# Performance work log

Measured on AMD Instinct MI355X. Metric: run time of the kernel, lower is better.

Reference implementation:

```python
import jax, jax.numpy as jnp
import numpy as np
from jax.ops import segment_sum, segment_max

N, E = 50000, 500000
D_IN, D_H, D_OUT = 128, 256, 40
BN_EPS = 1e-5


def setup_inputs() -> dict:
    key = jax.random.key(0)
    ks = jax.random.split(key, 16)
    g = lambda k, shape, fan: jax.random.normal(k, shape, jnp.float32) * (1.0 / np.sqrt(fan))
    inp = {
        "x": jax.random.normal(ks[0], (N, D_IN), jnp.float32),
        "edge_index": jax.random.randint(ks[1], (2, E), 0, N, jnp.int64),
        # GAT (heads=1)
        "W_gat": g(ks[2], (D_IN, D_H), D_IN),
        "att_src": g(ks[3], (D_H,), D_H),
        "att_dst": g(ks[4], (D_H,), D_H),
        "b_gat": jnp.zeros((D_H,), jnp.float32),
        # GIN MLP
        "W_gin1": g(ks[5], (D_IN, D_H), D_IN),
        "b_gin1": jnp.zeros((D_H,), jnp.float32),
        "W_gin2": g(ks[6], (D_H, D_H), D_H),
        "b_gin2": jnp.zeros((D_H,), jnp.float32),
        # GCN
        "W_gcn": g(ks[7], (D_IN, D_H), D_IN),
        "b_gcn": jnp.zeros((D_H,), jnp.float32),
        # BatchNorm1d(3*hidden)
        "gamma": jnp.ones((3 * D_H,), jnp.float32),
        "beta": jnp.zeros((3 * D_H,), jnp.float32),
        # head
        "W_lin": g(ks[8], (3 * D_H, D_H), 3 * D_H),
        "b_lin": jnp.zeros((D_H,), jnp.float32),
        "W_lin2": g(ks[9], (D_H, D_OUT), D_H),
        "b_lin2": jnp.zeros((D_OUT,), jnp.float32),
    }
    return inp


def _forward(x, edge_index, W_gat, att_src, att_dst, b_gat, W_gin1, b_gin1,
             W_gin2, b_gin2, W_gcn, b_gcn, gamma, beta, W_lin, b_lin, W_lin2, b_lin2):
    n = x.shape[0]
    src, dst = edge_index[0], edge_index[1]
    loop = jnp.arange(n, dtype=src.dtype)
    src_sl = jnp.concatenate([src, loop])  # edges + self-loops (GAT/GCN)
    dst_sl = jnp.concatenate([dst, loop])

    # ---- GATConv (1 head), messages src -> dst, softmax over dst ----
    xs = x @ W_gat                                   # [N, H]
    a = jax.nn.leaky_relu(xs @ att_src, negative_slope=0.2) if False else None
    e = (xs @ att_src)[src_sl] + (xs @ att_dst)[dst_sl]   # [E+N]
    e = jax.nn.leaky_relu(e, negative_slope=0.2)
    m = segment_max(e, dst_sl, num_segments=n)
    w = jnp.exp(e - m[dst_sl])
    denom = segment_sum(w, dst_sl, num_segments=n)
    alpha = w / denom[dst_sl]
    x_gat = segment_sum(alpha[:, None] * xs[src_sl], dst_sl, num_segments=n) + b_gat

    # ---- GINConv (eps=0): MLP(x + sum_neighbors x_j) ----
    agg = segment_sum(x[src], dst, num_segments=n)
    h = x + agg
    x_gin = jax.nn.relu(h @ W_gin1 + b_gin1) @ W_gin2 + b_gin2

    # ---- GCNConv: symmetric normalization with self-loops ----
    deg = segment_sum(jnp.ones_like(dst_sl, dtype=x.dtype), dst_sl, num_segments=n)
    dis = jax.lax.rsqrt(jnp.maximum(deg, 1.0))  # deg >= 1 due to self-loops
    norm = dis[src_sl] * dis[dst_sl]
    xw = x @ W_gcn
    x_gcn = segment_sum(norm[:, None] * xw[src_sl], dst_sl, num_segments=n) + b_gcn

    # ---- concat -> BN (training-mode batch stats) -> ReLU -> MLP head ----
    xc = jnp.concatenate([x_gat, x_gin, x_gcn], axis=1)  # [N, 3H]
    mu = jnp.mean(xc, axis=0)
    var = jnp.mean((xc - mu) ** 2, axis=0)
    xb = (xc - mu) * jax.lax.rsqrt(var + BN_EPS) * gamma + beta
    h2 = jax.nn.relu(jax.nn.relu(xb) @ W_lin + b_lin)
    return h2 @ W_lin2 + b_lin2


def reference(x, edge_index, W_gat, att_src, att_dst, b_gat, W_gin1, b_gin1,
              W_gin2, b_gin2, W_gcn, b_gcn, gamma, beta, W_lin, b_lin, W_lin2, b_lin2):
    return _forward(x, edge_index, W_gat, att_src, att_dst, b_gat, W_gin1, b_gin1,
                    W_gin2, b_gin2, W_gcn, b_gcn, gamma, beta, W_lin, b_lin, W_lin2, b_lin2)
```

## Files before the change

### kernel.cpp

```cpp
#include <hip/hip_runtime.h>
#include <math.h>

#define NN 50000
#define NE 500000

typedef __attribute__((ext_vector_type(8))) short short8;
typedef __attribute__((ext_vector_type(4))) float f32x4;

__device__ __forceinline__ float leaky02(float x) { return x > 0.f ? x : 0.2f * x; }
__device__ __forceinline__ ushort f2b(float f) {
    uint u = __float_as_uint(f);
    u += 0x7fffu + ((u >> 16) & 1u);
    return (ushort)(u >> 16);
}
__device__ __forceinline__ float b2f(ushort h) { return __uint_as_float(((uint)h) << 16); }
__device__ __forceinline__ float b2f_lo(uint w) { return __uint_as_float(w << 16); }
__device__ __forceinline__ float b2f_hi(uint w) { return __uint_as_float(w & 0xffff0000u); }
__device__ __forceinline__ uint pack2(float a, float b) {
    return (uint)f2b(a) | ((uint)f2b(b) << 16);
}

__global__ void mm_wt(const float* __restrict__ W, ushort* __restrict__ Wt, int K, int Nc)
{
    int idx = blockIdx.x * 256 + threadIdx.x;
    if (idx >= K * Nc) return;
    int n = idx / K, k = idx - n * K;
    Wt[idx] = f2b(W[(size_t)k * Nc + n]);
}

__global__ void mm_attvec(const float* __restrict__ W, const float* __restrict__ as_,
                          const float* __restrict__ ad_, float* __restrict__ va, float* __restrict__ vd)
{
    int i = threadIdx.x;
    const float* vec = (i < 128) ? as_ : ad_;
    int k = i & 127;
    float s = 0.f;
    for (int j = 0; j < 256; ++j) s += W[(size_t)k * 256 + j] * vec[j];
    if (i < 128) va[k] = s; else vd[k] = s;
}

__global__ __launch_bounds__(256) void mm_cvt_es(const float* __restrict__ x,
                                                 const float* __restrict__ va, const float* __restrict__ vd,
                                                 ushort* __restrict__ xb,
                                                 float* __restrict__ es, float* __restrict__ ed)
{
    int node = blockIdx.x * 4 + (threadIdx.x >> 6);
    int lane = threadIdx.x & 63;
    if (node >= NN) return;
    float2 xv = *(const float2*)(x + (size_t)node * 128 + lane * 2);
    float2 a = *(const float2*)(va + lane * 2);
    float2 b = *(const float2*)(vd + lane * 2);
    *(uint*)(xb + (size_t)node * 128 + lane * 2) = pack2(xv.x, xv.y);
    float s = xv.x * a.x + xv.y * a.y;
    float d = xv.x * b.x + xv.y * b.y;
    #pragma unroll
    for (int off = 32; off; off >>= 1) {
        s += __shfl_down(s, off);
        d += __shfl_down(d, off);
    }
    if (lane == 0) { es[node] = s; ed[node] = d; }
}

__global__ void mm_count(const int* __restrict__ dst, int* __restrict__ deg)
{
    int e = blockIdx.x * 256 + threadIdx.x;
    if (e >= NE) return;
    atomicAdd(&deg[dst[e]], 1);
}

__global__ __launch_bounds__(256) void mm_scan1(const int* __restrict__ deg, int* __restrict__ part)
{
    __shared__ int red[256];
    int i = blockIdx.x * 256 + threadIdx.x;
    red[threadIdx.x] = (i < NN) ? deg[i] : 0;
    __syncthreads();
    for (int off = 128; off; off >>= 1) {
        if (threadIdx.x < off) red[threadIdx.x] += red[threadIdx.x + off];
        __syncthreads();
    }
    if (threadIdx.x == 0) part[blockIdx.x] = red[0];
}

__global__ __launch_bounds__(256) void mm_scan2(int* __restrict__ part, int nb)
{
    __shared__ int tile[256];
    int t = threadIdx.x;
    int v = (t < nb) ? part[t] : 0;
    tile[t] = v; __syncthreads();
    for (int off = 1; off < 256; off <<= 1) {
        int a = (t >= off) ? tile[t - off] : 0;
        __syncthreads();
        tile[t] += a;
        __syncthreads();
    }
    if (t < nb) part[t] = tile[t] - v;
}

__global__ __launch_bounds__(256) void mm_scan3(const int* __restrict__ deg, const int* __restrict__ part,
                                                int* __restrict__ row_ptr, int* __restrict__ cursor)
{
    __shared__ int tile[256];
    int t = threadIdx.x;
    int i = blockIdx.x * 256 + t;
    int v = (i < NN) ? deg[i] : 0;
    tile[t] = v; __syncthreads();
    for (int off = 1; off < 256; off <<= 1) {
        int a = (t >= off) ? tile[t - off] : 0;
        __syncthreads();
        tile[t] += a;
        __syncthreads();
    }
    if (i < NN) {
        int ex = part[blockIdx.x] + tile[t] - v;
        row_ptr[i] = ex;
        cursor[i] = ex;
    }
    if (i == 0) row_ptr[NN] = NE;
}

__global__ void mm_fill(const int* __restrict__ src, const int* __restrict__ dst,
                        int* __restrict__ cursor, int* __restrict__ csr_src)
{
    int e = blockIdx.x * 256 + threadIdx.x;
    if (e >= NE) return;
    int pos = atomicAdd(&cursor[dst[e]], 1);
    csr_src[pos] = src[e];
}

__global__ void mm_dis(const int* __restrict__ row_ptr, float* __restrict__ dis)
{
    int i = blockIdx.x * 256 + threadIdx.x;
    if (i >= NN) return;
    dis[i] = rsqrtf((float)(row_ptr[i + 1] - row_ptr[i] + 1));
}

__global__ __launch_bounds__(256) void mm_node_agg(
    const int* __restrict__ row_ptr, const int* __restrict__ csr_src,
    const float* __restrict__ es, const float* __restrict__ ed,
    const float* __restrict__ dis,
    const ushort* __restrict__ xb, ushort* __restrict__ aggb)
{
    int d = blockIdx.x * 4 + (threadIdx.x >> 6);
    int lane = threadIdx.x & 63;
    if (d >= NN) return;
    int start = row_ptr[d], end = row_ptr[d + 1];
    float edd = ed[d], disd = dis[d];
    float selfv = leaky02(es[d] + edd);

    int myidx = -1; float myl = -3.0e38f, mynw = 0.f;
    if (start + lane < end) {
        myidx = csr_src[start + lane];
        myl = leaky02(es[myidx] + edd);
        mynw = dis[myidx] * disd;
    }
    float lmax = fmaxf(selfv, myl);
    for (int e = start + 64 + lane; e < end; e += 64)
        lmax = fmaxf(lmax, leaky02(es[csr_src[e]] + edd));
    #pragma unroll
    for (int off = 1; off < 64; off <<= 1) lmax = fmaxf(lmax, __shfl_xor(lmax, off));
    float m = lmax;

    float lsum = (myidx >= 0) ? __expf(myl - m) : 0.f;
    if (lane == 0) lsum += __expf(selfv - m);
    for (int e = start + 64 + lane; e < end; e += 64)
        lsum += __expf(leaky02(es[csr_src[e]] + edd) - m);
    #pragma unroll
    for (int off = 1; off < 64; off <<= 1) lsum += __shfl_xor(lsum, off);
    float inv = 1.f / lsum;
    float myal = __expf(myl - m) * inv;

    float aself = __expf(selfv - m) * inv;
    float d2 = disd * disd;
    uint wself = *(const uint*)(xb + (size_t)d * 128 + lane * 2);
    float x0 = b2f_lo(wself), x1 = b2f_hi(wself);
    float gat0 = aself * x0, gat1 = aself * x1;
    float gin0 = x0, gin1 = x1;
    float gcn0 = d2 * x0, gcn1 = d2 * x1;

    for (int base = start; base < end; base += 64) {
        int cnt = min(64, end - base);
        int bidx; float bal, bnw;
        if (base == start) { bidx = myidx; bal = myal; bnw = mynw; }
        else {
            bidx = -1; bal = 0.f; bnw = 0.f;
            if (base + lane < end) {
                bidx = csr_src[base + lane];
                bal = __expf(leaky02(es[bidx] + edd) - m) * inv;
                bnw = dis[bidx] * disd;
            }
        }
        int j = 0;
        for (; j + 4 <= cnt; j += 4) {
            int   s0 = __shfl(bidx, j),     s1 = __shfl(bidx, j + 1);
            int   s2 = __shfl(bidx, j + 2), s3 = __shfl(bidx, j + 3);
            float a0 = __shfl(bal, j),      a1 = __shfl(bal, j + 1);
            float a2 = __shfl(bal, j + 2),  a3 = __shfl(bal, j + 3);
            float n0 = __shfl(bnw, j),      n1 = __shfl(bnw, j + 1);
            float n2 = __shfl(bnw, j + 2),  n3 = __shfl(bnw, j + 3);
            uint w0 = *(const uint*)(xb + (size_t)s0 * 128 + lane * 2);
            uint w1 = *(const uint*)(xb + (size_t)s1 * 128 + lane * 2);
            uint w2 = *(const uint*)(xb + (size_t)s2 * 128 + lane * 2);
            uint w3 = *(const uint*)(xb + (size_t)s3 * 128 + lane * 2);
            float p0, p1;
            p0 = b2f_lo(w0); p1 = b2f_hi(w0);
            gat0 += a0 * p0; gat1 += a0 * p1; gin0 += p0; gin1 += p1; gcn0 += n0 * p0; gcn1 += n0 * p1;
            p0 = b2f_lo(w1); p1 = b2f_hi(w1);
            gat0 += a1 * p0; gat1 += a1 * p1; gin0 += p0; gin1 += p1; gcn0 += n1 * p0; gcn1 += n1 * p1;
            p0 = b2f_lo(w2); p1 = b2f_hi(w2);
            gat0 += a2 * p0; gat1 += a2 * p1; gin0 += p0; gin1 += p1; gcn0 += n2 * p0; gcn1 += n2 * p1;
            p0 = b2f_lo(w3); p1 = b2f_hi(w3);
            gat0 += a3 * p0; gat1 += a3 * p1; gin0 += p0; gin1 += p1; gcn0 += n3 * p0; gcn1 += n3 * p1;
        }
        for (; j < cnt; ++j) {
            int   s0 = __shfl(bidx, j);
            float a0 = __shfl(bal, j);
            float n0 = __shfl(bnw, j);
            uint w0 = *(const uint*)(xb + (size_t)s0 * 128 + lane * 2);
            float p0 = b2f_lo(w0), p1 = b2f_hi(w0);
            gat0 += a0 * p0; gat1 += a0 * p1; gin0 += p0; gin1 += p1; gcn0 += n0 * p0; gcn1 += n0 * p1;
        }
    }
    ushort* orow = aggb + (size_t)d * 384;
    *(uint*)(orow + lane * 2)       = pack2(gat0, gat1);
    *(uint*)(orow + 128 + lane * 2) = pack2(gin0, gin1);
    *(uint*)(orow + 256 + lane * 2) = pack2(gcn0, gcn1);
}

__global__ __launch_bounds__(256) void mm_gemm_bf(
    const ushort* __restrict__ A, int lda, const ushort* __restrict__ Bt,
    const float* __restrict__ bias, float* __restrict__ stats,
    ushort* __restrict__ Cb, int ldc,
    int M, int K, int relu)
{
    __shared__ ushort lds[16384];
    const int tid = threadIdx.x;
    const int wave = tid >> 6, lane = tid & 63;
    const int row0 = blockIdx.x * 128;
    const int col0 = blockIdx.y * 128;

    int arow0 = min(row0 + wave * 16 + (lane >> 2), M - 1);
    int arow1 = min(row0 + 64 + wave * 16 + (lane >> 2), M - 1);
    int brow0 = col0 + wave * 16 + (lane >> 2);
    int brow1 = col0 + 64 + wave * 16 + (lane >> 2);
    const ushort* pa0 = A + (size_t)arow0 * lda + (lane & 3) * 8;
    const ushort* pa1 = A + (size_t)arow1 * lda + (lane & 3) * 8;
    const ushort* pb0 = Bt + (size_t)brow0 * K + (lane & 3) * 8;
    const ushort* pb1 = Bt + (size_t)brow1 * K + (lane & 3) * 8;
    const int wr = (wave >> 1) * 64, wc = (wave & 1) * 64;

    f32x4 zero = {0.f, 0.f, 0.f, 0.f};
    f32x4 acc[4][4];
    #pragma unroll
    for (int m = 0; m < 4; ++m)
        #pragma unroll
        for (int n = 0; n < 4; ++n) acc[m][n] = zero;

    const int nt = K >> 5;

#define STAGE_BF(bufi) { \
    ushort* Lb = lds + (bufi) * 8192; \
    __builtin_amdgcn_global_load_lds((const __attribute__((address_space(1))) void*)pa0, \
        (__attribute__((address_space(3))) void*)(Lb + wave * 512), 16, 0, 0); \
    __builtin_amdgcn_global_load_lds((const __attribute__((address_space(1))) void*)pa1, \
        (__attribute__((address_space(3))) void*)(Lb + 2048 + wave * 512), 16, 0, 0); \
    __builtin_amdgcn_global_load_lds((const __attribute__((address_space(1))) void*)pb0, \
        (__attribute__((address_space(3))) void*)(Lb + 4096 + wave * 512), 16, 0, 0); \
    __builtin_amdgcn_global_load_lds((const __attribute__((address_space(1))) void*)pb1, \
        (__attribute__((address_space(3))) void*)(Lb + 6144 + wave * 512), 16, 0, 0); \
    pa0 += 32; pa1 += 32; pb0 += 32; pb1 += 32; }

    STAGE_BF(0);
    __syncthreads();
    for (int t = 0; t < nt; ++t) {
        int cur = t & 1;
        if (t + 1 < nt) STAGE_BF(cur ^ 1);
        const ushort* As = lds + cur * 8192;
        const ushort* Bs = As + 4096;
        short8 a[4], b[4];
        #pragma unroll
        for (int m = 0; m < 4; ++m)
            a[m] = *(const short8*)&As[(wr + m * 16 + (lane & 15)) * 32 + (lane >> 4) * 8];
        #pragma unroll
        for (int n = 0; n < 4; ++n)
            b[n] = *(const short8*)&Bs[(wc + n * 16 + (lane & 15)) * 32 + (lane >> 4) * 8];
        #pragma unroll
        for (int m = 0; m < 4; ++m)
            #pragma unroll
            for (int n = 0; n < 4; ++n)
                acc[m][n] = __builtin_amdgcn_mfma_f32_16x16x32_bf16(a[m], b[n], acc[m][n], 0, 0, 0);
        if (t + 1 < nt) __syncthreads();
    }
#undef STAGE_BF

    #pragma unroll
    for (int n = 0; n < 4; ++n) {
        int col = col0 + wc + n * 16 + (lane & 15);
        float bb = bias ? bias[col] : 0.f;
        float s_acc = 0.f, q_acc = 0.f;
        #pragma unroll
        for (int m = 0; m < 4; ++m) {
            int rb = row0 + wr + m * 16 + (lane >> 4) * 4;
            #pragma unroll
            for (int r = 0; r < 4; ++r) {
                int row = rb + r;
                if (row < M) {
                    float v = acc[m][n][r] + bb;
                    if (relu) v = fmaxf(v, 0.f);
                    Cb[(size_t)row * ldc + col] = f2b(v);
                    s_acc += v; q_acc += v * v;
                }
            }
        }
        if (stats) {
            s_acc += __shfl_xor(s_acc, 16); q_acc += __shfl_xor(q_acc, 16);
            s_acc += __shfl_xor(s_acc, 32); q_acc += __shfl_xor(q_acc, 32);
            if (lane < 16) {
                unsafeAtomicAdd(&stats[col], s_acc);
                unsafeAtomicAdd(&stats[768 + col], q_acc);
            }
        }
    }
}

__device__ __forceinline__ uint4 bn_relu_pack(uint4 w, const float* __restrict__ sc,
                                              const float* __restrict__ sh, int c)
{
    float4 sc0 = *(const float4*)(sc + c), sc1 = *(const float4*)(sc + c + 4);
    float4 sh0 = *(const float4*)(sh + c), sh1 = *(const float4*)(sh + c + 4);
    uint4 o;
    o.x = pack2(fmaxf(b2f_lo(w.x) * sc0.x + sh0.x, 0.f), fmaxf(b2f_hi(w.x) * sc0.y + sh0.y, 0.f));
    o.y = pack2(fmaxf(b2f_lo(w.y) * sc0.z + sh0.z, 0.f), fmaxf(b2f_hi(w.y) * sc0.w + sh0.w, 0.f));
    o.z = pack2(fmaxf(b2f_lo(w.z) * sc1.x + sh1.x, 0.f), fmaxf(b2f_hi(w.z) * sc1.y + sh1.y, 0.f));
    o.w = pack2(fmaxf(b2f_lo(w.w) * sc1.z + sh1.z, 0.f), fmaxf(b2f_hi(w.w) * sc1.w + sh1.w, 0.f));
    return o;
}

__global__ __launch_bounds__(256) void mm_gemm_bn(
    const ushort* __restrict__ A, const ushort* __restrict__ Bt,
    const float* __restrict__ bias,
    const float* __restrict__ sc, const float* __restrict__ sh,
    ushort* __restrict__ Cb, int ldc, int M)
{
    const int K = 768, lda = 768;
    __shared__ ushort lds[16384];
    const int tid = threadIdx.x;
    const int wave = tid >> 6, lane = tid & 63;
    const int row0 = blockIdx.x * 128;
    const int col0 = blockIdx.y * 128;

    int arow0 = min(row0 + wave * 16 + (lane >> 2), M - 1);
    int arow1 = min(row0 + 64 + wave * 16 + (lane >> 2), M - 1);
    int brow0 = col0 + wave * 16 + (lane >> 2);
    int brow1 = col0 + 64 + wave * 16 + (lane >> 2);
    const ushort* pa0 = A + (size_t)arow0 * lda + (lane & 3) * 8;
    const ushort* pa1 = A + (size_t)arow1 * lda + (lane & 3) * 8;
    const ushort* pb0 = Bt + (size_t)brow0 * K + (lane & 3) * 8;
    const ushort* pb1 = Bt + (size_t)brow1 * K + (lane & 3) * 8;
    const int wr = (wave >> 1) * 64, wc = (wave & 1) * 64;

    f32x4 zero = {0.f, 0.f, 0.f, 0.f};
    f32x4 acc[4][4];
    #pragma unroll
    for (int m = 0; m < 4; ++m)
        #pragma unroll
        for (int n = 0; n < 4; ++n) acc[m][n] = zero;

    const int nt = K >> 5;

#define STAGE_B(bufi) { \
    ushort* Lb = lds + (bufi) * 8192; \
    __builtin_amdgcn_global_load_lds((const __attribute__((address_space(1))) void*)pb0, \
        (__attribute__((address_space(3))) void*)(Lb + 4096 + wave * 512), 16, 0, 0); \
    __builtin_amdgcn_global_load_lds((const __attribute__((address_space(1))) void*)pb1, \
        (__attribute__((address_space(3))) void*)(Lb + 6144 + wave * 512), 16, 0, 0); \
    pb0 += 32; pb1 += 32; }

    {
        STAGE_B(0);
        uint4 w0 = *(const uint4*)pa0; uint4 w1 = *(const uint4*)pa1;
        pa0 += 32; pa1 += 32;
        int c = (lane & 3) * 8;
        uint4 oa = bn_relu_pack(w0, sc, sh, c);
        uint4 ob = bn_relu_pack(w1, sc, sh, c);
        *(uint4*)(lds + wave * 512 + lane * 8) = oa;
        *(uint4*)(lds + 2048 + wave * 512 + lane * 8) = ob;
    }
    __syncthreads();

    for (int t = 0; t < nt; ++t) {
        int cur = t & 1;
        uint4 w0n, w1n; int cn = 0;
        bool more = (t + 1 < nt);
        if (more) {
            STAGE_B(cur ^ 1);
            w0n = *(const uint4*)pa0; w1n = *(const uint4*)pa1;
            pa0 += 32; pa1 += 32;
            cn = (t + 1) * 32 + (lane & 3) * 8;
        }
        const ushort* As = lds + cur * 8192;
        const ushort* Bs = As + 4096;
        short8 a[4], b[4];
        #pragma unroll
        for (int m = 0; m < 4; ++m)
            a[m] = *(const short8*)&As[(wr + m * 16 + (lane & 15)) * 32 + (lane >> 4) * 8];
        #pragma unroll
        for (int n = 0; n < 4; ++n)
            b[n] = *(const short8*)&Bs[(wc + n * 16 + (lane & 15)) * 32 + (lane >> 4) * 8];
        #pragma unroll
        for (int m = 0; m < 4; ++m)
            #pragma unroll
            for (int n = 0; n < 4; ++n)
                acc[m][n] = __builtin_amdgcn_mfma_f32_16x16x32_bf16(a[m], b[n], acc[m][n], 0, 0, 0);
        if (more) {
            ushort* Ln = lds + (cur ^ 1) * 8192;
            uint4 oa = bn_relu_pack(w0n, sc, sh, cn);
            uint4 ob = bn_relu_pack(w1n, sc, sh, cn);
            *(uint4*)(Ln + wave * 512 + lane * 8) = oa;
            *(uint4*)(Ln + 2048 + wave * 512 + lane * 8) = ob;
            __syncthreads();
        }
    }
#undef STAGE_B

    #pragma unroll
    for (int n = 0; n < 4; ++n) {
        int col = col0 + wc + n * 16 + (lane & 15);
        float bb = bias[col];
        #pragma unroll
        for (int m = 0; m < 4; ++m) {
            int rb = row0 + wr + m * 16 + (lane >> 4) * 4;
            #pragma unroll
            for (int r = 0; r < 4; ++r) {
                int row = rb + r;
                if (row < M)
                    Cb[(size_t)row * ldc + col] = f2b(fmaxf(acc[m][n][r] + bb, 0.f));
            }
        }
    }
}

__global__ void mm_bn_fin(const float* __restrict__ sums, const float* __restrict__ gamma,
                          const float* __restrict__ beta,
                          float* __restrict__ scale, float* __restrict__ shift)
{
    int c = blockIdx.x * 256 + threadIdx.x;
    if (c >= 768) return;
    float inv = 1.f / (float)NN;
    float mu = sums[c] * inv;
    float ex2 = sums[768 + c] * inv;
    float var = fmaxf(ex2 - mu * mu, 0.f);
    float rs = rsqrtf(var + 1e-5f);
    float sc = gamma[c] * rs;
    scale[c] = sc;
    shift[c] = beta[c] - mu * sc;
}

__global__ __launch_bounds__(256) void mm_head2(const ushort* __restrict__ h2b, const float* __restrict__ W2,
                                                const float* __restrict__ b2, float* __restrict__ out)
{
    __shared__ float Ws[256 * 40];
    for (int i = threadIdx.x; i < 256 * 40; i += 256) Ws[i] = W2[i];
    __syncthreads();
    int row = blockIdx.x * 32 + (threadIdx.x >> 3);
    int cg = (threadIdx.x & 7) * 5;
    if (row >= NN) return;
    const ushort* hr = h2b + (size_t)row * 256;
    float acc[5] = {0, 0, 0, 0, 0};
    for (int k = 0; k < 256; k += 8) {
        uint4 w = *(const uint4*)(hr + k);
        float a0 = b2f_lo(w.x), a1 = b2f_hi(w.x), a2 = b2f_lo(w.y), a3 = b2f_hi(w.y);
        float a4 = b2f_lo(w.z), a5 = b2f_hi(w.z), a6 = b2f_lo(w.w), a7 = b2f_hi(w.w);
        #pragma unroll
        for (int j = 0; j < 5; ++j) {
            acc[j] += a0 * Ws[(k + 0) * 40 + cg + j] + a1 * Ws[(k + 1) * 40 + cg + j]
                    + a2 * Ws[(k + 2) * 40 + cg + j] + a3 * Ws[(k + 3) * 40 + cg + j]
                    + a4 * Ws[(k + 4) * 40 + cg + j] + a5 * Ws[(k + 5) * 40 + cg + j]
                    + a6 * Ws[(k + 6) * 40 + cg + j] + a7 * Ws[(k + 7) * 40 + cg + j];
        }
    }
    #pragma unroll
    for (int j = 0; j < 5; ++j) out[(size_t)row * 40 + cg + j] = acc[j] + b2[cg + j];
}

extern "C" void kernel_launch(void* const* d_in, const int* in_sizes, int n_in,
                              void* d_out, int out_size, void* d_ws, size_t ws_size,
                              hipStream_t stream)
{
    const float* x      = (const float*)d_in[0];
    const int*   ei     = (const int*)d_in[1];
    const float* W_gat  = (const float*)d_in[2];
    const float* att_s  = (const float*)d_in[3];
    const float* att_d  = (const float*)d_in[4];
    const float* b_gat  = (const float*)d_in[5];
    const float* W_gin1 = (const float*)d_in[6];
    const float* b_gin1 = (const float*)d_in[7];
    const float* W_gin2 = (const float*)d_in[8];
    const float* b_gin2 = (const float*)d_in[9];
    const float* W_gcn  = (const float*)d_in[10];
    const float* b_gcn  = (const float*)d_in[11];
    const float* gamma  = (const float*)d_in[12];
    const float* beta   = (const float*)d_in[13];
    const float* W_lin  = (const float*)d_in[14];
    const float* b_lin  = (const float*)d_in[15];
    const float* W_lin2 = (const float*)d_in[16];
    const float* b_lin2 = (const float*)d_in[17];
    const int* src = ei;
    const int* dst = ei + NE;
    float* out = (float*)d_out;

    float* ws = (float*)d_ws;
    size_t off = 0;
    ushort* xb      = (ushort*)(ws + off); off += (size_t)NN * 64;
    ushort* aggb    = (ushort*)(ws + off); off += (size_t)NN * 192;
    ushort* hid_b   = (ushort*)(ws + off); off += (size_t)NN * 128;
    ushort* xcb     = (ushort*)(ws + off); off += (size_t)NN * 384;
    float* es       = ws + off; off += NN;
    float* ed       = ws + off; off += NN;
    float* dis      = ws + off; off += NN;
    float* va       = ws + off; off += 128;
    float* vd       = ws + off; off += 128;
    float* bnsum    = ws + off; off += 1536;
    float* bscale   = ws + off; off += 768;
    float* bshift   = ws + off; off += 768;
    ushort* wt_gat  = (ushort*)(ws + off); off += 128 * 256 / 2;
    ushort* wt_gin1 = (ushort*)(ws + off); off += 128 * 256 / 2;
    ushort* wt_gin2 = (ushort*)(ws + off); off += 256 * 256 / 2;
    ushort* wt_gcn  = (ushort*)(ws + off); off += 128 * 256 / 2;
    ushort* wt_lin  = (ushort*)(ws + off); off += 768 * 256 / 2;
    int* part       = (int*)(ws + off); off += 256;
    int* row_ptr    = (int*)(ws + off); off += NN + 1;
    int* cursor     = (int*)(ws + off); off += NN;
    int* csr_src    = (int*)(ws + off); off += NE;

    dim3 blk(256);
    dim3 gemm_grid((NN + 127) / 128, 2);
    const int NB = (NN + 255) / 256;

    hipMemsetAsync(bnsum, 0, 1536 * sizeof(float), stream);
    hipMemsetAsync(cursor, 0, NN * sizeof(int), stream);

    mm_wt<<<(128 * 256 + 255) / 256, blk, 0, stream>>>(W_gat, wt_gat, 128, 256);
    mm_wt<<<(128 * 256 + 255) / 256, blk, 0, stream>>>(W_gin1, wt_gin1, 128, 256);
    mm_wt<<<(256 * 256 + 255) / 256, blk, 0, stream>>>(W_gin2, wt_gin2, 256, 256);
    mm_wt<<<(128 * 256 + 255) / 256, blk, 0, stream>>>(W_gcn, wt_gcn, 128, 256);
    mm_wt<<<(768 * 256 + 255) / 256, blk, 0, stream>>>(W_lin, wt_lin, 768, 256);
    mm_attvec<<<1, blk, 0, stream>>>(W_gat, att_s, att_d, va, vd);

    mm_cvt_es<<<(NN + 3) / 4, blk, 0, stream>>>(x, va, vd, xb, es, ed);

    mm_count<<<(NE + 255) / 256, blk, 0, stream>>>(dst, cursor);
    mm_scan1<<<NB, blk, 0, stream>>>(cursor, part);
    mm_scan2<<<1, blk, 0, stream>>>(part, NB);
    mm_scan3<<<NB, blk, 0, stream>>>(cursor, part, row_ptr, cursor);
    mm_dis<<<(NN + 255) / 256, blk, 0, stream>>>(row_ptr, dis);
    mm_fill<<<(NE + 255) / 256, blk, 0, stream>>>(src, dst, cursor, csr_src);

    mm_node_agg<<<(NN + 3) / 4, blk, 0, stream>>>(row_ptr, csr_src, es, ed, dis, xb, aggb);

    mm_gemm_bf<<<gemm_grid, blk, 0, stream>>>(aggb,       384, wt_gat,  b_gat,  bnsum,       xcb,       768, NN, 128, 0);
    mm_gemm_bf<<<gemm_grid, blk, 0, stream>>>(aggb + 128, 384, wt_gin1, b_gin1, nullptr,     hid_b,     256, NN, 128, 1);
    mm_gemm_bf<<<gemm_grid, blk, 0, stream>>>(hid_b,      256, wt_gin2, b_gin2, bnsum + 256, xcb + 256, 768, NN, 256, 0);
    mm_gemm_bf<<<gemm_grid, blk, 0, stream>>>(aggb + 256, 384, wt_gcn,  b_gcn,  bnsum + 512, xcb + 512, 768, NN, 128, 0);

    mm_bn_fin<<<3, blk, 0, stream>>>(bnsum, gamma, beta, bscale, bshift);

    mm_gemm_bn<<<gemm_grid, blk, 0, stream>>>(xcb, wt_lin, b_lin, bscale, bshift, hid_b, 256, NN);
    mm_head2<<<(NN + 31) / 32, blk, 0, stream>>>(hid_b, W_lin2, b_lin2, out);
}
```

Before: 419.2 us.

## Batch three GEMMs into one launch and relax LDS pipeline barriers

Folds the GAT, GIN1 and GCN projection GEMMs into one grid-z-indexed launch, cutting launch overhead and tail effects. Both GEMM kernels replace __syncthreads with explicit partial s_waitcnt vmcnt(4) plus raw s_barrier, so the next tile's async LDS loads can stay in flight while the current tile computes. The BN GEMM also caches the scale and shift vectors in shared memory and issues the A-row global loads earlier. Hand-written waitcnt counts are fragile and must exactly match the number of outstanding loads, or the kernel reads stale LDS data.

```diff
diff --git a/kernel.cpp b/kernel.cpp
--- a/kernel.cpp
+++ b/kernel.cpp
@@ -226,13 +226,12 @@
     *(uint*)(orow + 256 + lane * 2) = pack2(gcn0, gcn1);
 }
 
-__global__ __launch_bounds__(256) void mm_gemm_bf(
+__device__ __forceinline__ void gemm_core(
     const ushort* __restrict__ A, int lda, const ushort* __restrict__ Bt,
     const float* __restrict__ bias, float* __restrict__ stats,
-    ushort* __restrict__ Cb, int ldc,
-    int M, int K, int relu)
-{
-    __shared__ ushort lds[16384];
+    ushort* __restrict__ Cb, int ldc, int M, int K, int relu,
+    ushort* lds)
+{
     const int tid = threadIdx.x;
     const int wave = tid >> 6, lane = tid & 63;
     const int row0 = blockIdx.x * 128;
@@ -257,7 +256,7 @@
 
     const int nt = K >> 5;
 
-#define STAGE_BF(bufi) { \
+#define STAGE_C(bufi) { \
     ushort* Lb = lds + (bufi) * 8192; \
     __builtin_amdgcn_global_load_lds((const __attribute__((address_space(1))) void*)pa0, \
         (__attribute__((address_space(3))) void*)(Lb + wave * 512), 16, 0, 0); \
@@ -269,11 +268,16 @@
         (__attribute__((address_space(3))) void*)(Lb + 6144 + wave * 512), 16, 0, 0); \
     pa0 += 32; pa1 += 32; pb0 += 32; pb1 += 32; }
 
-    STAGE_BF(0);
-    __syncthreads();
+    STAGE_C(0);
     for (int t = 0; t < nt; ++t) {
         int cur = t & 1;
-        if (t + 1 < nt) STAGE_BF(cur ^ 1);
+        if (t + 1 < nt) {
+            STAGE_C(cur ^ 1);
+            asm volatile("s_waitcnt vmcnt(4) lgkmcnt(0)" ::: "memory");
+        } else {
+            asm volatile("s_waitcnt vmcnt(0) lgkmcnt(0)" ::: "memory");
+        }
+        __builtin_amdgcn_s_barrier();
         const ushort* As = lds + cur * 8192;
         const ushort* Bs = As + 4096;
         short8 a[4], b[4];
@@ -288,9 +292,9 @@
             #pragma unroll
             for (int n = 0; n < 4; ++n)
                 acc[m][n] = __builtin_amdgcn_mfma_f32_16x16x32_bf16(a[m], b[n], acc[m][n], 0, 0, 0);
-        if (t + 1 < nt) __syncthreads();
-    }
-#undef STAGE_BF
+        if (t + 1 < nt) __builtin_amdgcn_s_barrier();
+    }
+#undef STAGE_C
 
     #pragma unroll
     for (int n = 0; n < 4; ++n) {
@@ -322,16 +326,37 @@
     }
 }
 
-__device__ __forceinline__ uint4 bn_relu_pack(uint4 w, const float* __restrict__ sc,
-                                              const float* __restrict__ sh, int c)
-{
-    float4 sc0 = *(const float4*)(sc + c), sc1 = *(const float4*)(sc + c + 4);
-    float4 sh0 = *(const float4*)(sh + c), sh1 = *(const float4*)(sh + c + 4);
+__global__ __launch_bounds__(256) void mm_gemm3(
+    const ushort* __restrict__ aggb,
+    const ushort* __restrict__ wt_gat, const ushort* __restrict__ wt_gin1, const ushort* __restrict__ wt_gcn,
+    const float* __restrict__ b_gat, const float* __restrict__ b_gin1, const float* __restrict__ b_gcn,
+    float* __restrict__ bnsum,
+    ushort* __restrict__ xcb, ushort* __restrict__ hid_b)
+{
+    __shared__ ushort lds[16384];
+    const ushort* A; const ushort* Bt; const float* bias; float* stats; ushort* Cb; int ldc; int relu;
+    if (blockIdx.z == 0)      { A = aggb;       Bt = wt_gat;  bias = b_gat;  stats = bnsum;       Cb = xcb;       ldc = 768; relu = 0; }
+    else if (blockIdx.z == 1) { A = aggb + 128; Bt = wt_gin1; bias = b_gin1; stats = nullptr;     Cb = hid_b;     ldc = 256; relu = 1; }
+    else                      { A = aggb + 256; Bt = wt_gcn;  bias = b_gcn;  stats = bnsum + 512; Cb = xcb + 512; ldc = 768; relu = 0; }
+    gemm_core(A, 384, Bt, bias, stats, Cb, ldc, NN, 128, relu, lds);
+}
+
+__global__ __launch_bounds__(256) void mm_gemm_bf(
+    const ushort* __restrict__ A, int lda, const ushort* __restrict__ Bt,
+    const float* __restrict__ bias, float* __restrict__ stats,
+    ushort* __restrict__ Cb, int ldc, int M, int K, int relu)
+{
+    __shared__ ushort lds[16384];
+    gemm_core(A, lda, Bt, bias, stats, Cb, ldc, M, K, relu, lds);
+}
+
+__device__ __forceinline__ uint4 bn_relu_pack_l(uint4 w, const float* sc, const float* sh, int c)
+{
     uint4 o;
-    o.x = pack2(fmaxf(b2f_lo(w.x) * sc0.x + sh0.x, 0.f), fmaxf(b2f_hi(w.x) * sc0.y + sh0.y, 0.f));
-    o.y = pack2(fmaxf(b2f_lo(w.y) * sc0.z + sh0.z, 0.f), fmaxf(b2f_hi(w.y) * sc0.w + sh0.w, 0.f));
-    o.z = pack2(fmaxf(b2f_lo(w.z) * sc1.x + sh1.x, 0.f), fmaxf(b2f_hi(w.z) * sc1.y + sh1.y, 0.f));
-    o.w = pack2(fmaxf(b2f_lo(w.w) * sc1.z + sh1.z, 0.f), fmaxf(b2f_hi(w.w) * sc1.w + sh1.w, 0.f));
+    o.x = pack2(fmaxf(b2f_lo(w.x) * sc[c + 0] + sh[c + 0], 0.f), fmaxf(b2f_hi(w.x) * sc[c + 1] + sh[c + 1], 0.f));
+    o.y = pack2(fmaxf(b2f_lo(w.y) * sc[c + 2] + sh[c + 2], 0.f), fmaxf(b2f_hi(w.y) * sc[c + 3] + sh[c + 3], 0.f));
+    o.z = pack2(fmaxf(b2f_lo(w.z) * sc[c + 4] + sh[c + 4], 0.f), fmaxf(b2f_hi(w.z) * sc[c + 5] + sh[c + 5], 0.f));
+    o.w = pack2(fmaxf(b2f_lo(w.w) * sc[c + 6] + sh[c + 6], 0.f), fmaxf(b2f_hi(w.w) * sc[c + 7] + sh[c + 7], 0.f));
     return o;
 }
 
@@ -343,7 +368,10 @@
 {
     const int K = 768, lda = 768;
     __shared__ ushort lds[16384];
+    __shared__ float sc_l[768], sh_l[768];
     const int tid = threadIdx.x;
+    for (int i = tid; i < 768; i += 256) { sc_l[i] = sc[i]; sh_l[i] = sh[i]; }
+
     const int wave = tid >> 6, lane = tid & 63;
     const int row0 = blockIdx.x * 128;
     const int col0 = blockIdx.y * 128;
@@ -375,28 +403,29 @@
         (__attribute__((address_space(3))) void*)(Lb + 6144 + wave * 512), 16, 0, 0); \
     pb0 += 32; pb1 += 32; }
 
+    uint4 w0 = *(const uint4*)pa0, w1 = *(const uint4*)pa1;
+    pa0 += 32; pa1 += 32;
+    STAGE_B(0);
+    __syncthreads();
     {
-        STAGE_B(0);
-        uint4 w0 = *(const uint4*)pa0; uint4 w1 = *(const uint4*)pa1;
-        pa0 += 32; pa1 += 32;
         int c = (lane & 3) * 8;
-        uint4 oa = bn_relu_pack(w0, sc, sh, c);
-        uint4 ob = bn_relu_pack(w1, sc, sh, c);
-        *(uint4*)(lds + wave * 512 + lane * 8) = oa;
-        *(uint4*)(lds + 2048 + wave * 512 + lane * 8) = ob;
-    }
-    __syncthreads();
+        *(uint4*)(lds + wave * 512 + lane * 8) = bn_relu_pack_l(w0, sc_l, sh_l, c);
+        *(uint4*)(lds + 2048 + wave * 512 + lane * 8) = bn_relu_pack_l(w1, sc_l, sh_l, c);
+    }
 
     for (int t = 0; t < nt; ++t) {
         int cur = t & 1;
-        uint4 w0n, w1n; int cn = 0;
         bool more = (t + 1 < nt);
+        uint4 w0n, w1n;
         if (more) {
-            STAGE_B(cur ^ 1);
             w0n = *(const uint4*)pa0; w1n = *(const uint4*)pa1;
             pa0 += 32; pa1 += 32;
-            cn = (t + 1) * 32 + (lane & 3) * 8;
-        }
+            STAGE_B(cur ^ 1);
+            asm volatile("s_waitcnt vmcnt(4) lgkmcnt(0)" ::: "memory");
+        } else {
+            asm volatile("s_waitcnt vmcnt(0) lgkmcnt(0)" ::: "memory");
+        }
+        __builtin_amdgcn_s_barrier();
         const ushort* As = lds + cur * 8192;
         const ushort* Bs = As + 4096;
         short8 a[4], b[4];
@@ -412,12 +441,11 @@
             for (int n = 0; n < 4; ++n)
                 acc[m][n] = __builtin_amdgcn_mfma_f32_16x16x32_bf16(a[m], b[n], acc[m][n], 0, 0, 0);
         if (more) {
+            int c = (t + 1) * 32 + (lane & 3) * 8;
             ushort* Ln = lds + (cur ^ 1) * 8192;
-            uint4 oa = bn_relu_pack(w0n, sc, sh, cn);
-            uint4 ob = bn_relu_pack(w1n, sc, sh, cn);
-            *(uint4*)(Ln + wave * 512 + lane * 8) = oa;
-            *(uint4*)(Ln + 2048 + wave * 512 + lane * 8) = ob;
-            __syncthreads();
+            *(uint4*)(Ln + wave * 512 + lane * 8) = bn_relu_pack_l(w0n, sc_l, sh_l, c);
+            *(uint4*)(Ln + 2048 + wave * 512 + lane * 8) = bn_relu_pack_l(w1n, sc_l, sh_l, c);
+            __builtin_amdgcn_s_barrier();
         }
     }
 #undef STAGE_B
@@ -534,6 +562,7 @@
 
     dim3 blk(256);
     dim3 gemm_grid((NN + 127) / 128, 2);
+    dim3 gemm_grid3((NN + 127) / 128, 2, 3);
     const int NB = (NN + 255) / 256;
 
     hipMemsetAsync(bnsum, 0, 1536 * sizeof(float), stream);
@@ -557,10 +586,10 @@
 
     mm_node_agg<<<(NN + 3) / 4, blk, 0, stream>>>(row_ptr, csr_src, es, ed, dis, xb, aggb);
 
-    mm_gemm_bf<<<gemm_grid, blk, 0, stream>>>(aggb,       384, wt_gat,  b_gat,  bnsum,       xcb,       768, NN, 128, 0);
-    mm_gemm_bf<<<gemm_grid, blk, 0, stream>>>(aggb + 128, 384, wt_gin1, b_gin1, nullptr,     hid_b,     256, NN, 128, 1);
-    mm_gemm_bf<<<gemm_grid, blk, 0, stream>>>(hid_b,      256, wt_gin2, b_gin2, bnsum + 256, xcb + 256, 768, NN, 256, 0);
-    mm_gemm_bf<<<gemm_grid, blk, 0, stream>>>(aggb + 256, 384, wt_gcn,  b_gcn,  bnsum + 512, xcb + 512, 768, NN, 128, 0);
+    mm_gemm3<<<gemm_grid3, blk, 0, stream>>>(aggb, wt_gat, wt_gin1, wt_gcn,
+                                             b_gat, b_gin1, b_gcn, bnsum, xcb, hid_b);
+    mm_gemm_bf<<<gemm_grid, blk, 0, stream>>>(hid_b, 256, wt_gin2, b_gin2, bnsum + 256,
+                                              xcb + 256, 768, NN, 256, 0);
 
     mm_bn_fin<<<3, blk, 0, stream>>>(bnsum, gamma, beta, bscale, bshift);
 
```

Result: faster. 377.1 us (-10.0%).
